# Performance work log

Measured on AMD Instinct MI355X. Metric: run time of the kernel, lower is better.

The kernel has to match this reference:

```python
import jax, jax.numpy as jnp
import numpy as np

E, T = 8, 256          # n_experts, chunk length
IN, OUT = 1024, 1024   # input_size, output_size
D1, D2 = 32, 32        # nearest factors of IN
DO1, DO2 = 32, 32      # nearest factors of OUT
B, L = 8, 2048
LOSS_COEF = 1e-5


def setup_inputs() -> dict:
    key = jax.random.key(0)
    ks = jax.random.split(key, 12)
    eyeE = lambda d, k: (jnp.broadcast_to(jnp.eye(d, dtype=jnp.float32), (E, d, d))
                         + 0.01 * jax.random.normal(k, (E, d, d), jnp.float32))
    return {
        "x": jax.random.normal(ks[0], (B, L, IN), jnp.float32),
        "w_gate": 0.02 * jax.random.normal(ks[1], (IN, E), jnp.float32),
        "weight": 0.02 * jax.random.normal(ks[2], (E, OUT, IN), jnp.float32),
        "bias": 0.02 * jax.random.normal(ks[3], (E, OUT), jnp.float32),
        "res_weight": 0.02 * jax.random.normal(ks[4], (OUT, IN), jnp.float32),
        "res_bias": 0.02 * jax.random.normal(ks[5], (1, OUT), jnp.float32),
        "curve1_in": eyeE(D1, ks[6]),
        "curve2_in": eyeE(D2, ks[7]),
        "curve1_out": eyeE(DO1, ks[8]),
        "curve2_out": eyeE(DO2, ks[9]),
        "curve1_bias": eyeE(DO1, ks[10]),
        "curve2_bias": eyeE(DO2, ks[11]),
    }


def _cv_squared(v):
    v = v.astype(jnp.float32)
    return jnp.var(v, ddof=1) / (jnp.mean(v) ** 2 + 1e-10)


def reference(x, w_gate, weight, bias, res_weight, res_bias,
              curve1_in, curve2_in, curve1_out, curve2_out,
              curve1_bias, curve2_bias):
    Bx, Lx, d = x.shape
    N = Lx // T
    BN = Bx * N
    xr = x.reshape(BN, T, d)

    # --- gating (eval mode, ties_merging forces k = n_experts -> plain softmax) ---
    logits = xr.mean(axis=1) @ w_gate            # [BN, E]
    gates = jax.nn.softmax(logits, axis=1)        # [BN, E]
    load = (gates > 0).sum(axis=0).astype(jnp.float32)
    importance = gates.sum(axis=0)
    loss = (_cv_squared(importance) + _cv_squared(load)) * LOSS_COEF

    # --- roll gates by one segment, keeping each sample's first chunk (detached) ---
    e_first = jax.lax.stop_gradient(gates.reshape(Bx, N, E)[:, 0])
    g = jnp.roll(gates, 1, axis=0).reshape(Bx, N, E)
    g = g.at[:, 0].set(e_first).reshape(BN, E)

    # --- Kronecker curve-factored expert weight merge ---
    rw = (weight - res_weight).reshape(E, DO1, DO2, D1, D2)
    rw = jnp.einsum('bij,bjklm->biklm', curve1_out, rw)
    rw = jnp.einsum('bik,bjklm->bjilm', curve2_out, rw)
    rw = jnp.einsum('bil,bjklm->bjkim', curve1_in, rw)
    rw = jnp.einsum('bim,bjklm->bjkli', curve2_in, rw)
    rw = rw.reshape(E, OUT, IN)
    expert_weights = res_weight + jnp.einsum('be,eoi->boi', g, rw)  # [BN, O, I]

    y = jnp.einsum('bij,bkj->bik', xr, expert_weights)  # [BN, T, O]

    # --- curve-factored expert bias merge ---
    rb = (bias - res_bias).reshape(E, DO1, DO2)
    rb = jnp.einsum('bki,bij->bkj', curve1_bias, rb)      # [E, DO1, DO2]
    rb = jnp.einsum('bkj,bij->bik', curve2_bias, rb)      # [E, DO1, DO2]
    rb = rb.reshape(E, OUT)
    expert_bias = res_bias + jnp.einsum('be,eo->bo', g, rb)  # [BN, O]

    y = (y + expert_bias[:, None, :]).reshape(Bx, Lx, OUT)
    return y, loss
```

## Files before the change

kernel.cpp:

```cpp
#include <hip/hip_runtime.h>
#include <cstdint>

typedef __bf16 bf16x8 __attribute__((ext_vector_type(8)));
typedef float  f32x4  __attribute__((ext_vector_type(4)));
typedef unsigned int u32x4 __attribute__((ext_vector_type(4)));
using u16 = unsigned short;

struct alignas(8) u16x4 { u16 x, y, z, w; };

__device__ __forceinline__ u16 f2bf(float f) {
  unsigned u = __builtin_bit_cast(unsigned, f);
  u = (u + 0x7FFFu + ((u >> 16) & 1u)) >> 16;
  return (u16)u;
}
__device__ __forceinline__ float bf2f(u16 u) {
  unsigned v = ((unsigned)u) << 16;
  return __builtin_bit_cast(float, v);
}

static constexpr size_t OFF_XBF  = 0;
static constexpr size_t OFF_EW   = 33554432;
static constexpr size_t OFF_T2   = 33554432;
static constexpr size_t OFF_PM   = 67108864;
static constexpr size_t OFF_RW   = 167772160;
static constexpr size_t OFF_LG   = 201326592;
static constexpr size_t OFF_G    = 201588736;
static constexpr size_t OFF_RB   = 201592832;
static constexpr size_t WS_NEED  = 201887744;

__global__ __launch_bounds__(256) void k_means(const float* __restrict__ x,
                                               float* __restrict__ pm,
                                               u16* __restrict__ xbf) {
  int b = blockIdx.x, q = blockIdx.y, tid = threadIdx.x;
  const float* xb = x + (size_t)b * 262144 + (size_t)q * 16384 + tid * 4;
  u16* xo = xbf + (size_t)b * 262144 + (size_t)q * 16384 + tid * 4;
  float s0 = 0.f, s1 = 0.f, s2 = 0.f, s3 = 0.f;
#pragma unroll
  for (int t = 0; t < 16; ++t) {
    float4 v = *(const float4*)(xb + t * 1024);
    s0 += v.x; s1 += v.y; s2 += v.z; s3 += v.w;
    u16x4 o; o.x = f2bf(v.x); o.y = f2bf(v.y); o.z = f2bf(v.z); o.w = f2bf(v.w);
    *(u16x4*)(xo + t * 1024) = o;
  }
  float4 sv; sv.x = s0; sv.y = s1; sv.z = s2; sv.w = s3;
  *(float4*)(pm + ((size_t)b * 16 + q) * 1024 + tid * 4) = sv;
}

__global__ __launch_bounds__(256) void k_redlogits(const float* __restrict__ pm,
                                                   const float* __restrict__ w_gate,
                                                   float* __restrict__ logits) {
  __shared__ float red[4][8];
  int b = blockIdx.x, tid = threadIdx.x;
  const float* p = pm + (size_t)b * 16384 + tid * 4;
  float4 s = {0.f, 0.f, 0.f, 0.f};
#pragma unroll
  for (int q = 0; q < 16; ++q) {
    float4 v = *(const float4*)(p + q * 1024);
    s.x += v.x; s.y += v.y; s.z += v.z; s.w += v.w;
  }
  int i0 = tid * 4;
  float acc[8];
#pragma unroll
  for (int e = 0; e < 8; ++e) {
    acc[e] = s.x * w_gate[(i0 + 0) * 8 + e] + s.y * w_gate[(i0 + 1) * 8 + e]
           + s.z * w_gate[(i0 + 2) * 8 + e] + s.w * w_gate[(i0 + 3) * 8 + e];
  }
#pragma unroll
  for (int off = 32; off >= 1; off >>= 1)
#pragma unroll
    for (int e = 0; e < 8; ++e) acc[e] += __shfl_down(acc[e], off, 64);
  int wv = tid >> 6;
  if ((tid & 63) == 0)
#pragma unroll
    for (int e = 0; e < 8; ++e) red[wv][e] = acc[e];
  __syncthreads();
  if (tid < 8)
    logits[b * 8 + tid] =
        (red[0][tid] + red[1][tid] + red[2][tid] + red[3][tid]) * (1.f / 256.f);
}

__global__ __launch_bounds__(64) void k_gatefin(const float* __restrict__ logits,
                                                float* __restrict__ g,
                                                float* __restrict__ loss_out) {
  __shared__ float gates[64][8];
  __shared__ float imp[8];
  int b = threadIdx.x;
  {
    float lg[8];
#pragma unroll
    for (int j = 0; j < 8; ++j) lg[j] = logits[b * 8 + j];
    float mx = lg[0];
#pragma unroll
    for (int j = 1; j < 8; ++j) mx = fmaxf(mx, lg[j]);
    float s = 0.f, ex[8];
#pragma unroll
    for (int j = 0; j < 8; ++j) { ex[j] = expf(lg[j] - mx); s += ex[j]; }
    float inv = 1.f / s;
#pragma unroll
    for (int j = 0; j < 8; ++j) gates[b][j] = ex[j] * inv;
  }
  __syncthreads();
  if (b < 8) {
    float s = 0.f;
    for (int bb = 0; bb < 64; ++bb) s += gates[bb][b];
    imp[b] = s;
  }
  __syncthreads();
  if (b == 0) {
    float mean = 0.f;
#pragma unroll
    for (int j = 0; j < 8; ++j) mean += imp[j];
    mean *= (1.f / 8.f);
    float var = 0.f;
#pragma unroll
    for (int j = 0; j < 8; ++j) { float d = imp[j] - mean; var += d * d; }
    var *= (1.f / 7.f);
    loss_out[0] = (var / (mean * mean + 1e-10f)) * 1e-5f;
  }
  __syncthreads();
  {
    int src = ((b & 7) == 0) ? b : b - 1;
#pragma unroll
    for (int j = 0; j < 8; ++j) g[b * 8 + j] = gates[src][j];
  }
}

__global__ __launch_bounds__(256) void k_mergeA(const float* __restrict__ W,
                                                const float* __restrict__ R,
                                                const float* __restrict__ c1o,
                                                const float* __restrict__ c2o,
                                                u16* __restrict__ T2t) {
  __shared__ float dw[8 * 1024];
  __shared__ float m1[1024], m2[1024];
  int e = blockIdx.y, c0 = blockIdx.x * 8, tid = threadIdx.x;
  const float* We = W + (size_t)e * 1048576;
  for (int idx = tid; idx < 1024; idx += 256) {
    m1[idx] = c1o[e * 1024 + idx];
    m2[idx] = c2o[e * 1024 + idx];
  }
  {
    int r = tid >> 1, h = (tid & 1) * 4;
#pragma unroll
    for (int i = 0; i < 8; ++i) {
      int row = r + i * 128;
      const float4 wv = *(const float4*)(We + (size_t)row * 1024 + c0 + h);
      const float4 rv = *(const float4*)(R + (size_t)row * 1024 + c0 + h);
      dw[(h + 0) * 1024 + row] = wv.x - rv.x;
      dw[(h + 1) * 1024 + row] = wv.y - rv.y;
      dw[(h + 2) * 1024 + row] = wv.z - rv.z;
      dw[(h + 3) * 1024 + row] = wv.w - rv.w;
    }
  }
  __syncthreads();
  int i1 = tid & 31, c = tid >> 5;
  const float* dwc = dw + c * 1024;
  float U[32];
#pragma unroll
  for (int k = 0; k < 32; ++k) U[k] = 0.f;
  for (int j = 0; j < 32; ++j) {
    float cj = m1[i1 * 32 + j];
    const float4* rowp = (const float4*)(dwc + j * 32);
#pragma unroll
    for (int k4 = 0; k4 < 8; ++k4) {
      float4 v = rowp[k4];
      U[k4 * 4 + 0] += cj * v.x; U[k4 * 4 + 1] += cj * v.y;
      U[k4 * 4 + 2] += cj * v.z; U[k4 * 4 + 3] += cj * v.w;
    }
  }
  u16* obase = T2t + (size_t)e * 1048576 + (size_t)(c0 + c) * 1024 + i1 * 32;
#pragma unroll
  for (int g4 = 0; g4 < 8; ++g4) {
    float s[4];
#pragma unroll
    for (int q = 0; q < 4; ++q) {
      const float4* m2r = (const float4*)(m2 + (g4 * 4 + q) * 32);
      float acc = 0.f;
#pragma unroll
      for (int k4 = 0; k4 < 8; ++k4) {
        float4 mv = m2r[k4];
        acc += mv.x * U[k4 * 4 + 0] + mv.y * U[k4 * 4 + 1]
             + mv.z * U[k4 * 4 + 2] + mv.w * U[k4 * 4 + 3];
      }
      s[q] = acc;
    }
    u16x4 o4; o4.x = f2bf(s[0]); o4.y = f2bf(s[1]); o4.z = f2bf(s[2]); o4.w = f2bf(s[3]);
    *(u16x4*)(obase + g4 * 4) = o4;
  }
}

__global__ __launch_bounds__(256) void k_mergeB(const u16* __restrict__ T2t,
                                                const float* __restrict__ c1i,
                                                const float* __restrict__ c2i,
                                                u16* __restrict__ RWbf) {
  __shared__ float t2[8 * 1024];
  __shared__ float m1[1024], m2[1024];
  int e = blockIdx.y, o0 = blockIdx.x * 8, tid = threadIdx.x;
  const u16* Te = T2t + (size_t)e * 1048576;
  for (int idx = tid; idx < 1024; idx += 256) {
    m1[idx] = c1i[e * 1024 + idx];
    m2[idx] = c2i[e * 1024 + idx];
  }
  {
    int r = tid >> 1, h = (tid & 1) * 4;
#pragma unroll
    for (int i = 0; i < 8; ++i) {
      int row = r + i * 128;
      const u16x4 tv = *(const u16x4*)(Te + (size_t)row * 1024 + o0 + h);
      t2[(h + 0) * 1024 + row] = bf2f(tv.x);
      t2[(h + 1) * 1024 + row] = bf2f(tv.y);
      t2[(h + 2) * 1024 + row] = bf2f(tv.z);
      t2[(h + 3) * 1024 + row] = bf2f(tv.w);
    }
  }
  __syncthreads();
  int i1 = tid & 31, oc = tid >> 5;
  const float* t2c = t2 + oc * 1024;
  float A[32];
#pragma unroll
  for (int m = 0; m < 32; ++m) A[m] = 0.f;
  for (int l = 0; l < 32; ++l) {
    float cl = m1[i1 * 32 + l];
    const float4* rowp = (const float4*)(t2c + l * 32);
#pragma unroll
    for (int m4 = 0; m4 < 8; ++m4) {
      float4 v = rowp[m4];
      A[m4 * 4 + 0] += cl * v.x; A[m4 * 4 + 1] += cl * v.y;
      A[m4 * 4 + 2] += cl * v.z; A[m4 * 4 + 3] += cl * v.w;
    }
  }
  u16* obase = RWbf + ((size_t)e * 1024 + o0 + oc) * 1024 + i1 * 32;
#pragma unroll
  for (int g4 = 0; g4 < 8; ++g4) {
    float s[4];
#pragma unroll
    for (int q = 0; q < 4; ++q) {
      const float4* m2r = (const float4*)(m2 + (g4 * 4 + q) * 32);
      float acc = 0.f;
#pragma unroll
      for (int m4 = 0; m4 < 8; ++m4) {
        float4 mv = m2r[m4];
        acc += mv.x * A[m4 * 4 + 0] + mv.y * A[m4 * 4 + 1]
             + mv.z * A[m4 * 4 + 2] + mv.w * A[m4 * 4 + 3];
      }
      s[q] = acc;
    }
    u16x4 o4; o4.x = f2bf(s[0]); o4.y = f2bf(s[1]); o4.z = f2bf(s[2]); o4.w = f2bf(s[3]);
    *(u16x4*)(obase + g4 * 4) = o4;
  }
}

__global__ __launch_bounds__(256) void k_rb(const float* __restrict__ bias,
                                            const float* __restrict__ res_bias,
                                            const float* __restrict__ c1b,
                                            const float* __restrict__ c2b,
                                            float* __restrict__ rb) {
  __shared__ float rb0[32][33], rb1[32][33], m1[32][32], m2[32][32];
  int e = blockIdx.x, tid = threadIdx.x;
  for (int idx = tid; idx < 1024; idx += 256) {
    int i = idx >> 5, j = idx & 31;
    rb0[i][j] = bias[e * 1024 + idx] - res_bias[idx];
    m1[i][j] = c1b[e * 1024 + idx];
    m2[i][j] = c2b[e * 1024 + idx];
  }
  __syncthreads();
  for (int idx = tid; idx < 1024; idx += 256) {
    int p = idx >> 5, j = idx & 31;
    float s = 0.f;
#pragma unroll
    for (int i = 0; i < 32; ++i) s += m1[p][i] * rb0[i][j];
    rb1[p][j] = s;
  }
  __syncthreads();
  for (int idx = tid; idx < 1024; idx += 256) {
    int p = idx >> 5, q = idx & 31;
    float s = 0.f;
#pragma unroll
    for (int j = 0; j < 32; ++j) s += m2[q][j] * rb1[p][j];
    rb[e * 1024 + idx] = s;
  }
}

__global__ __launch_bounds__(256) void k_combine(const u16* __restrict__ RWbf,
                                                 const float* __restrict__ R,
                                                 const float* __restrict__ g,
                                                 u16* __restrict__ EW) {
  __shared__ float gs[512];
  int o = blockIdx.x, tid = threadIdx.x;
  for (int idx = tid; idx < 512; idx += 256) gs[idx] = g[idx];
  __syncthreads();
  int i0 = tid * 4;
  float4 r4 = *(const float4*)(R + (size_t)o * 1024 + i0);
  float4 w[8];
#pragma unroll
  for (int e = 0; e < 8; ++e) {
    u16x4 t = *(const u16x4*)(RWbf + (size_t)e * 1048576 + (size_t)o * 1024 + i0);
    w[e].x = bf2f(t.x); w[e].y = bf2f(t.y); w[e].z = bf2f(t.z); w[e].w = bf2f(t.w);
  }
  for (int b = 0; b < 64; ++b) {
    float a0 = r4.x, a1 = r4.y, a2 = r4.z, a3 = r4.w;
#pragma unroll
    for (int e = 0; e < 8; ++e) {
      float ge = gs[b * 8 + e];
      a0 += ge * w[e].x; a1 += ge * w[e].y; a2 += ge * w[e].z; a3 += ge * w[e].w;
    }
    u16x4 u; u.x = f2bf(a0); u.y = f2bf(a1); u.z = f2bf(a2); u.w = f2bf(a3);
    *(u16x4*)(EW + (size_t)b * 1048576 + (size_t)o * 1024 + i0) = u;
  }
}

__global__ __launch_bounds__(512) void k_gemm(const u16* __restrict__ Xb,
                                              const u16* __restrict__ EW,
                                              const float* __restrict__ rb,
                                              const float* __restrict__ res_b,
                                              const float* __restrict__ g,
                                              float* __restrict__ Y) {
  __shared__ alignas(16) u16 As[2][256 * 64];
  __shared__ alignas(16) u16 Bs[2][256 * 64];
  int hw = blockIdx.x;
  int xcd = hw & 7;
  int b  = xcd * 8 + (hw >> 5);
  int nt = (hw >> 3) & 3;
  int t0 = b * 256, o0 = nt * 256;
  int tid = threadIdx.x, lane = tid & 63, wv = tid >> 6;
  int wr = wv >> 2, wc = wv & 3;
  f32x4 acc[8][4] = {};
  const u16* aG = Xb + (size_t)t0 * 1024;
  const u16* bG = EW + (size_t)b * 1048576 + (size_t)o0 * 1024;
  int srow = tid >> 3;
  int kcol = (tid & 7) << 3;
  int lr = lane & 15;
  int sx = lr & 7;
  u32x4 la[4], lb[4];
#pragma unroll
  for (int iss = 0; iss < 4; ++iss) {
    int r = srow + iss * 64;
    la[iss] = *(const u32x4*)(aG + (size_t)r * 1024 + kcol);
    lb[iss] = *(const u32x4*)(bG + (size_t)r * 1024 + kcol);
  }
  for (int kt = 0; kt < 16; ++kt) {
    int cur = kt & 1;
#pragma unroll
    for (int iss = 0; iss < 4; ++iss) {
      int r = srow + iss * 64;
      int wcl = (((tid & 7) ^ (r & 7)) << 3);
      *(u32x4*)&As[cur][r * 64 + wcl] = la[iss];
      *(u32x4*)&Bs[cur][r * 64 + wcl] = lb[iss];
    }
    __syncthreads();
    if (kt < 15) {
      int k0n = (kt + 1) << 6;
#pragma unroll
      for (int iss = 0; iss < 4; ++iss) {
        int r = srow + iss * 64;
        la[iss] = *(const u32x4*)(aG + (size_t)r * 1024 + k0n + kcol);
        lb[iss] = *(const u32x4*)(bG + (size_t)r * 1024 + k0n + kcol);
      }
    }
#pragma unroll
    for (int kk = 0; kk < 2; ++kk) {
      int c16 = kk * 4 + (lane >> 4);
      int cp = ((c16 ^ sx) << 3);
      bf16x8 af[8], bfr[4];
#pragma unroll
      for (int mi = 0; mi < 8; ++mi)
        af[mi] = *(const bf16x8*)&As[cur][(wr * 128 + mi * 16 + lr) * 64 + cp];
#pragma unroll
      for (int ni = 0; ni < 4; ++ni)
        bfr[ni] = *(const bf16x8*)&Bs[cur][(wc * 64 + ni * 16 + lr) * 64 + cp];
#pragma unroll
      for (int mi = 0; mi < 8; ++mi)
#pragma unroll
        for (int ni = 0; ni < 4; ++ni)
          acc[mi][ni] = __builtin_amdgcn_mfma_f32_16x16x32_bf16(af[mi], bfr[ni], acc[mi][ni], 0, 0, 0);
    }
  }
  float ge[8];
#pragma unroll
  for (int e = 0; e < 8; ++e) ge[e] = g[b * 8 + e];
  int rbase = (lane >> 4) << 2;
#pragma unroll
  for (int ni = 0; ni < 4; ++ni) {
    int o = o0 + wc * 64 + ni * 16 + lr;
    float ebv = res_b[o];
#pragma unroll
    for (int e = 0; e < 8; ++e) ebv += ge[e] * rb[e * 1024 + o];
#pragma unroll
    for (int mi = 0; mi < 8; ++mi) {
      int trow = t0 + wr * 128 + mi * 16 + rbase;
      float* yp = Y + (size_t)trow * 1024 + o;
      yp[0]    = acc[mi][ni][0] + ebv;
      yp[1024] = acc[mi][ni][1] + ebv;
      yp[2048] = acc[mi][ni][2] + ebv;
      yp[3072] = acc[mi][ni][3] + ebv;
    }
  }
}

extern "C" void kernel_launch(void* const* d_in, const int* in_sizes, int n_in,
                              void* d_out, int out_size, void* d_ws, size_t ws_size,
                              hipStream_t stream) {
  const float* x      = (const float*)d_in[0];
  const float* w_gate = (const float*)d_in[1];
  const float* weight = (const float*)d_in[2];
  const float* bias   = (const float*)d_in[3];
  const float* res_w  = (const float*)d_in[4];
  const float* res_b  = (const float*)d_in[5];
  const float* c1i    = (const float*)d_in[6];
  const float* c2i    = (const float*)d_in[7];
  const float* c1o    = (const float*)d_in[8];
  const float* c2o    = (const float*)d_in[9];
  const float* c1b    = (const float*)d_in[10];
  const float* c2b    = (const float*)d_in[11];
  float* y = (float*)d_out;

  if (ws_size < WS_NEED) return;

  char* wsb = (char*)d_ws;
  u16*   xbf   = (u16*)(wsb + OFF_XBF);
  u16*   EW    = (u16*)(wsb + OFF_EW);
  u16*   T2t   = (u16*)(wsb + OFF_T2);
  float* pm    = (float*)(wsb + OFF_PM);
  u16*   RWbf  = (u16*)(wsb + OFF_RW);
  float* lgts  = (float*)(wsb + OFF_LG);
  float* g     = (float*)(wsb + OFF_G);
  float* rb    = (float*)(wsb + OFF_RB);

  k_means    <<<dim3(64, 16), 256, 0, stream>>>(x, pm, xbf);
  k_redlogits<<<64, 256, 0, stream>>>(pm, w_gate, lgts);
  k_gatefin  <<<1, 64, 0, stream>>>(lgts, g, y + 16777216);
  k_mergeA   <<<dim3(128, 8), 256, 0, stream>>>(weight, res_w, c1o, c2o, T2t);
  k_mergeB   <<<dim3(128, 8), 256, 0, stream>>>(T2t, c1i, c2i, RWbf);
  k_rb       <<<8, 256, 0, stream>>>(bias, res_b, c1b, c2b, rb);
  k_combine  <<<1024, 256, 0, stream>>>(RWbf, res_w, g, EW);
  k_gemm     <<<256, 512, 0, stream>>>(xbf, EW, rb, res_b, g, y);
}
```

Measured before the change: 232.5 us.

## Fold gating and bias-merge kernels into merge kernels; use 1024-thread GEMM blocks

The logits reduction and the bias curve merge now run as an extra block column inside k_mergeA, and the softmax, loss and gate roll run inside an extra block of k_mergeB. This removes three separate small kernel launches and the serial gaps between them. Separately, the GEMM now launches 16 waves per block, each computing a 64x64 sub-tile instead of 128x64. That halves accumulator registers per thread and spreads the tile loads over more threads, with more waves contending for the same shared-memory tiles in exchange.

```diff
diff --git a/kernel.cpp b/kernel.cpp
--- a/kernel.cpp
+++ b/kernel.cpp
@@ -46,93 +46,79 @@
   *(float4*)(pm + ((size_t)b * 16 + q) * 1024 + tid * 4) = sv;
 }
 
-__global__ __launch_bounds__(256) void k_redlogits(const float* __restrict__ pm,
-                                                   const float* __restrict__ w_gate,
-                                                   float* __restrict__ logits) {
-  __shared__ float red[4][8];
-  int b = blockIdx.x, tid = threadIdx.x;
-  const float* p = pm + (size_t)b * 16384 + tid * 4;
-  float4 s = {0.f, 0.f, 0.f, 0.f};
-#pragma unroll
-  for (int q = 0; q < 16; ++q) {
-    float4 v = *(const float4*)(p + q * 1024);
-    s.x += v.x; s.y += v.y; s.z += v.z; s.w += v.w;
-  }
-  int i0 = tid * 4;
-  float acc[8];
-#pragma unroll
-  for (int e = 0; e < 8; ++e) {
-    acc[e] = s.x * w_gate[(i0 + 0) * 8 + e] + s.y * w_gate[(i0 + 1) * 8 + e]
-           + s.z * w_gate[(i0 + 2) * 8 + e] + s.w * w_gate[(i0 + 3) * 8 + e];
-  }
-#pragma unroll
-  for (int off = 32; off >= 1; off >>= 1)
-#pragma unroll
-    for (int e = 0; e < 8; ++e) acc[e] += __shfl_down(acc[e], off, 64);
-  int wv = tid >> 6;
-  if ((tid & 63) == 0)
-#pragma unroll
-    for (int e = 0; e < 8; ++e) red[wv][e] = acc[e];
-  __syncthreads();
-  if (tid < 8)
-    logits[b * 8 + tid] =
-        (red[0][tid] + red[1][tid] + red[2][tid] + red[3][tid]) * (1.f / 256.f);
-}
-
-__global__ __launch_bounds__(64) void k_gatefin(const float* __restrict__ logits,
-                                                float* __restrict__ g,
-                                                float* __restrict__ loss_out) {
-  __shared__ float gates[64][8];
-  __shared__ float imp[8];
-  int b = threadIdx.x;
-  {
-    float lg[8];
-#pragma unroll
-    for (int j = 0; j < 8; ++j) lg[j] = logits[b * 8 + j];
-    float mx = lg[0];
-#pragma unroll
-    for (int j = 1; j < 8; ++j) mx = fmaxf(mx, lg[j]);
-    float s = 0.f, ex[8];
-#pragma unroll
-    for (int j = 0; j < 8; ++j) { ex[j] = expf(lg[j] - mx); s += ex[j]; }
-    float inv = 1.f / s;
-#pragma unroll
-    for (int j = 0; j < 8; ++j) gates[b][j] = ex[j] * inv;
-  }
-  __syncthreads();
-  if (b < 8) {
-    float s = 0.f;
-    for (int bb = 0; bb < 64; ++bb) s += gates[bb][b];
-    imp[b] = s;
-  }
-  __syncthreads();
-  if (b == 0) {
-    float mean = 0.f;
-#pragma unroll
-    for (int j = 0; j < 8; ++j) mean += imp[j];
-    mean *= (1.f / 8.f);
-    float var = 0.f;
-#pragma unroll
-    for (int j = 0; j < 8; ++j) { float d = imp[j] - mean; var += d * d; }
-    var *= (1.f / 7.f);
-    loss_out[0] = (var / (mean * mean + 1e-10f)) * 1e-5f;
-  }
-  __syncthreads();
-  {
-    int src = ((b & 7) == 0) ? b : b - 1;
-#pragma unroll
-    for (int j = 0; j < 8; ++j) g[b * 8 + j] = gates[src][j];
-  }
-}
-
 __global__ __launch_bounds__(256) void k_mergeA(const float* __restrict__ W,
                                                 const float* __restrict__ R,
                                                 const float* __restrict__ c1o,
                                                 const float* __restrict__ c2o,
-                                                u16* __restrict__ T2t) {
+                                                u16* __restrict__ T2t,
+                                                const float* __restrict__ pm,
+                                                const float* __restrict__ w_gate,
+                                                float* __restrict__ logits,
+                                                const float* __restrict__ bias,
+                                                const float* __restrict__ res_bias,
+                                                const float* __restrict__ c1b,
+                                                const float* __restrict__ c2b,
+                                                float* __restrict__ rb) {
+  int e = blockIdx.y, bx = blockIdx.x, tid = threadIdx.x;
+  if (bx == 128) {
+    __shared__ float red[4][8];
+    for (int c = 0; c < 8; ++c) {
+      int b = e * 8 + c;
+      const float* p = pm + (size_t)b * 16384 + tid * 4;
+      float4 s = {0.f, 0.f, 0.f, 0.f};
+#pragma unroll
+      for (int q = 0; q < 16; ++q) {
+        float4 v = *(const float4*)(p + q * 1024);
+        s.x += v.x; s.y += v.y; s.z += v.z; s.w += v.w;
+      }
+      int i0 = tid * 4;
+      float acc[8];
+#pragma unroll
+      for (int e2 = 0; e2 < 8; ++e2) {
+        acc[e2] = s.x * w_gate[(i0 + 0) * 8 + e2] + s.y * w_gate[(i0 + 1) * 8 + e2]
+                + s.z * w_gate[(i0 + 2) * 8 + e2] + s.w * w_gate[(i0 + 3) * 8 + e2];
+      }
+#pragma unroll
+      for (int off = 32; off >= 1; off >>= 1)
+#pragma unroll
+        for (int e2 = 0; e2 < 8; ++e2) acc[e2] += __shfl_down(acc[e2], off, 64);
+      if ((tid & 63) == 0)
+#pragma unroll
+        for (int e2 = 0; e2 < 8; ++e2) red[tid >> 6][e2] = acc[e2];
+      __syncthreads();
+      if (tid < 8)
+        logits[b * 8 + tid] =
+            (red[0][tid] + red[1][tid] + red[2][tid] + red[3][tid]) * (1.f / 256.f);
+      __syncthreads();
+    }
+    __shared__ float rb0[32][33], rb1[32][33], m1b[32][32], m2b[32][32];
+    for (int idx = tid; idx < 1024; idx += 256) {
+      int i = idx >> 5, j = idx & 31;
+      rb0[i][j] = bias[e * 1024 + idx] - res_bias[idx];
+      m1b[i][j] = c1b[e * 1024 + idx];
+      m2b[i][j] = c2b[e * 1024 + idx];
+    }
+    __syncthreads();
+    for (int idx = tid; idx < 1024; idx += 256) {
+      int p = idx >> 5, j = idx & 31;
+      float s = 0.f;
+#pragma unroll
+      for (int i = 0; i < 32; ++i) s += m1b[p][i] * rb0[i][j];
+      rb1[p][j] = s;
+    }
+    __syncthreads();
+    for (int idx = tid; idx < 1024; idx += 256) {
+      int p = idx >> 5, q = idx & 31;
+      float s = 0.f;
+#pragma unroll
+      for (int j = 0; j < 32; ++j) s += m2b[q][j] * rb1[p][j];
+      rb[e * 1024 + idx] = s;
+    }
+    return;
+  }
   __shared__ float dw[8 * 1024];
   __shared__ float m1[1024], m2[1024];
-  int e = blockIdx.y, c0 = blockIdx.x * 8, tid = threadIdx.x;
+  int c0 = bx * 8;
   const float* We = W + (size_t)e * 1048576;
   for (int idx = tid; idx < 1024; idx += 256) {
     m1[idx] = c1o[e * 1024 + idx];
@@ -191,10 +177,58 @@
 __global__ __launch_bounds__(256) void k_mergeB(const u16* __restrict__ T2t,
                                                 const float* __restrict__ c1i,
                                                 const float* __restrict__ c2i,
-                                                u16* __restrict__ RWbf) {
+                                                u16* __restrict__ RWbf,
+                                                const float* __restrict__ logits,
+                                                float* __restrict__ g,
+                                                float* __restrict__ loss_out) {
+  int e = blockIdx.y, bx = blockIdx.x, tid = threadIdx.x;
+  if (bx == 128) {
+    if (e != 0) return;
+    __shared__ float gates[64][8];
+    __shared__ float imp[8];
+    if (tid < 64) {
+      float lg[8];
+#pragma unroll
+      for (int j = 0; j < 8; ++j) lg[j] = logits[tid * 8 + j];
+      float mx = lg[0];
+#pragma unroll
+      for (int j = 1; j < 8; ++j) mx = fmaxf(mx, lg[j]);
+      float s = 0.f, ex[8];
+#pragma unroll
+      for (int j = 0; j < 8; ++j) { ex[j] = expf(lg[j] - mx); s += ex[j]; }
+      float inv = 1.f / s;
+#pragma unroll
+      for (int j = 0; j < 8; ++j) gates[tid][j] = ex[j] * inv;
+    }
+    __syncthreads();
+    if (tid < 8) {
+      float s = 0.f;
+      for (int bb = 0; bb < 64; ++bb) s += gates[bb][tid];
+      imp[tid] = s;
+    }
+    __syncthreads();
+    if (tid == 0) {
+      float mean = 0.f;
+#pragma unroll
+      for (int j = 0; j < 8; ++j) mean += imp[j];
+      mean *= (1.f / 8.f);
+      float var = 0.f;
+#pragma unroll
+      for (int j = 0; j < 8; ++j) { float d = imp[j] - mean; var += d * d; }
+      var *= (1.f / 7.f);
+      loss_out[0] = (var / (mean * mean + 1e-10f)) * 1e-5f;
+    }
+    __syncthreads();
+    if (tid < 64) {
+      int src = ((tid & 7) == 0) ? tid : tid - 1;
+#pragma unroll
+      for (int j = 0; j < 8; ++j) g[tid * 8 + j] = gates[src][j];
+    }
+    return;
+  }
   __shared__ float t2[8 * 1024];
   __shared__ float m1[1024], m2[1024];
-  int e = blockIdx.y, o0 = blockIdx.x * 8, tid = threadIdx.x;
+  int o0 = bx * 8;
   const u16* Te = T2t + (size_t)e * 1048576;
   for (int idx = tid; idx < 1024; idx += 256) {
     m1[idx] = c1i[e * 1024 + idx];
@@ -246,37 +280,6 @@
     }
     u16x4 o4; o4.x = f2bf(s[0]); o4.y = f2bf(s[1]); o4.z = f2bf(s[2]); o4.w = f2bf(s[3]);
     *(u16x4*)(obase + g4 * 4) = o4;
-  }
-}
-
-__global__ __launch_bounds__(256) void k_rb(const float* __restrict__ bias,
-                                            const float* __restrict__ res_bias,
-                                            const float* __restrict__ c1b,
-                                            const float* __restrict__ c2b,
-                                            float* __restrict__ rb) {
-  __shared__ float rb0[32][33], rb1[32][33], m1[32][32], m2[32][32];
-  int e = blockIdx.x, tid = threadIdx.x;
-  for (int idx = tid; idx < 1024; idx += 256) {
-    int i = idx >> 5, j = idx & 31;
-    rb0[i][j] = bias[e * 1024 + idx] - res_bias[idx];
-    m1[i][j] = c1b[e * 1024 + idx];
-    m2[i][j] = c2b[e * 1024 + idx];
-  }
-  __syncthreads();
-  for (int idx = tid; idx < 1024; idx += 256) {
-    int p = idx >> 5, j = idx & 31;
-    float s = 0.f;
-#pragma unroll
-    for (int i = 0; i < 32; ++i) s += m1[p][i] * rb0[i][j];
-    rb1[p][j] = s;
-  }
-  __syncthreads();
-  for (int idx = tid; idx < 1024; idx += 256) {
-    int p = idx >> 5, q = idx & 31;
-    float s = 0.f;
-#pragma unroll
-    for (int j = 0; j < 32; ++j) s += m2[q][j] * rb1[p][j];
-    rb[e * 1024 + idx] = s;
   }
 }
 
@@ -308,12 +311,12 @@
   }
 }
 
-__global__ __launch_bounds__(512) void k_gemm(const u16* __restrict__ Xb,
-                                              const u16* __restrict__ EW,
-                                              const float* __restrict__ rb,
-                                              const float* __restrict__ res_b,
-                                              const float* __restrict__ g,
-                                              float* __restrict__ Y) {
+__global__ __launch_bounds__(1024) void k_gemm(const u16* __restrict__ Xb,
+                                               const u16* __restrict__ EW,
+                                               const float* __restrict__ rb,
+                                               const float* __restrict__ res_b,
+                                               const float* __restrict__ g,
+                                               float* __restrict__ Y) {
   __shared__ alignas(16) u16 As[2][256 * 64];
   __shared__ alignas(16) u16 Bs[2][256 * 64];
   int hw = blockIdx.x;
@@ -323,25 +326,25 @@
   int t0 = b * 256, o0 = nt * 256;
   int tid = threadIdx.x, lane = tid & 63, wv = tid >> 6;
   int wr = wv >> 2, wc = wv & 3;
-  f32x4 acc[8][4] = {};
+  f32x4 acc[4][4] = {};
   const u16* aG = Xb + (size_t)t0 * 1024;
   const u16* bG = EW + (size_t)b * 1048576 + (size_t)o0 * 1024;
   int srow = tid >> 3;
   int kcol = (tid & 7) << 3;
   int lr = lane & 15;
   int sx = lr & 7;
-  u32x4 la[4], lb[4];
-#pragma unroll
-  for (int iss = 0; iss < 4; ++iss) {
-    int r = srow + iss * 64;
+  u32x4 la[2], lb[2];
+#pragma unroll
+  for (int iss = 0; iss < 2; ++iss) {
+    int r = srow + iss * 128;
     la[iss] = *(const u32x4*)(aG + (size_t)r * 1024 + kcol);
     lb[iss] = *(const u32x4*)(bG + (size_t)r * 1024 + kcol);
   }
   for (int kt = 0; kt < 16; ++kt) {
     int cur = kt & 1;
 #pragma unroll
-    for (int iss = 0; iss < 4; ++iss) {
-      int r = srow + iss * 64;
+    for (int iss = 0; iss < 2; ++iss) {
+      int r = srow + iss * 128;
       int wcl = (((tid & 7) ^ (r & 7)) << 3);
       *(u32x4*)&As[cur][r * 64 + wcl] = la[iss];
       *(u32x4*)&Bs[cur][r * 64 + wcl] = lb[iss];
@@ -350,8 +353,8 @@
     if (kt < 15) {
       int k0n = (kt + 1) << 6;
 #pragma unroll
-      for (int iss = 0; iss < 4; ++iss) {
-        int r = srow + iss * 64;
+      for (int iss = 0; iss < 2; ++iss) {
+        int r = srow + iss * 128;
         la[iss] = *(const u32x4*)(aG + (size_t)r * 1024 + k0n + kcol);
         lb[iss] = *(const u32x4*)(bG + (size_t)r * 1024 + k0n + kcol);
       }
@@ -360,15 +363,15 @@
     for (int kk = 0; kk < 2; ++kk) {
       int c16 = kk * 4 + (lane >> 4);
       int cp = ((c16 ^ sx) << 3);
-      bf16x8 af[8], bfr[4];
-#pragma unroll
-      for (int mi = 0; mi < 8; ++mi)
-        af[mi] = *(const bf16x8*)&As[cur][(wr * 128 + mi * 16 + lr) * 64 + cp];
+      bf16x8 af[4], bfr[4];
+#pragma unroll
+      for (int mi = 0; mi < 4; ++mi)
+        af[mi] = *(const bf16x8*)&As[cur][(wr * 64 + mi * 16 + lr) * 64 + cp];
 #pragma unroll
       for (int ni = 0; ni < 4; ++ni)
         bfr[ni] = *(const bf16x8*)&Bs[cur][(wc * 64 + ni * 16 + lr) * 64 + cp];
 #pragma unroll
-      for (int mi = 0; mi < 8; ++mi)
+      for (int mi = 0; mi < 4; ++mi)
 #pragma unroll
         for (int ni = 0; ni < 4; ++ni)
           acc[mi][ni] = __builtin_amdgcn_mfma_f32_16x16x32_bf16(af[mi], bfr[ni], acc[mi][ni], 0, 0, 0);
@@ -385,8 +388,8 @@
 #pragma unroll
     for (int e = 0; e < 8; ++e) ebv += ge[e] * rb[e * 1024 + o];
 #pragma unroll
-    for (int mi = 0; mi < 8; ++mi) {
-      int trow = t0 + wr * 128 + mi * 16 + rbase;
+    for (int mi = 0; mi < 4; ++mi) {
+      int trow = t0 + wr * 64 + mi * 16 + rbase;
       float* yp = Y + (size_t)trow * 1024 + o;
       yp[0]    = acc[mi][ni][0] + ebv;
       yp[1024] = acc[mi][ni][1] + ebv;
@@ -425,12 +428,12 @@
   float* g     = (float*)(wsb + OFF_G);
   float* rb    = (float*)(wsb + OFF_RB);
 
-  k_means    <<<dim3(64, 16), 256, 0, stream>>>(x, pm, xbf);
-  k_redlogits<<<64, 256, 0, stream>>>(pm, w_gate, lgts);
-  k_gatefin  <<<1, 64, 0, stream>>>(lgts, g, y + 16777216);
-  k_mergeA   <<<dim3(128, 8), 256, 0, stream>>>(weight, res_w, c1o, c2o, T2t);
-  k_mergeB   <<<dim3(128, 8), 256, 0, stream>>>(T2t, c1i, c2i, RWbf);
-  k_rb       <<<8, 256, 0, stream>>>(bias, res_b, c1b, c2b, rb);
-  k_combine  <<<1024, 256, 0, stream>>>(RWbf, res_w, g, EW);
-  k_gemm     <<<256, 512, 0, stream>>>(xbf, EW, rb, res_b, g, y);
-}
+  k_means   <<<dim3(64, 16), 256, 0, stream>>>(x, pm, xbf);
+  k_mergeA  <<<dim3(129, 8), 256, 0, stream>>>(weight, res_w, c1o, c2o, T2t,
+                                               pm, w_gate, lgts,
+                                               bias, res_b, c1b, c2b, rb);
+  k_mergeB  <<<dim3(129, 8), 256, 0, stream>>>(T2t, c1i, c2i, RWbf,
+                                               lgts, g, y + 16777216);
+  k_combine <<<1024, 256, 0, stream>>>(RWbf, res_w, g, EW);
+  k_gemm    <<<256, 1024, 0, stream>>>(xbf, EW, rb, res_b, g, y);
+}
```

Result: no change. 235.3 us (+1.2%).
